# Optimization experiments

Measured on AMD Instinct MI355X. Metric: run time of the kernel, lower is better.

The kernel has to match this reference:

```python
import jax, jax.numpy as jnp
import numpy as np

D = 512
H = 8
DK = D // H
FF = 4 * D
EPS = 1e-5
NEG = -1.0e9


def _layernorm(x, g, b):
    mu = jnp.mean(x, axis=-1, keepdims=True)
    var = jnp.mean((x - mu) ** 2, axis=-1, keepdims=True)
    return (x - mu) * jax.lax.rsqrt(var + EPS) * g + b


def setup_inputs() -> dict:
    key = jax.random.key(0)
    ks = jax.random.split(key, 16)
    B, S = 4, 2048
    x = jax.random.normal(ks[0], (B, S, D), dtype=jnp.float32)
    # causal mask, broadcastable to [B, H, S, S]; mask==0 -> blocked
    mask = jnp.tril(jnp.ones((S, S), dtype=jnp.int32))[None, None]
    s = 1.0 / np.sqrt(D)
    sf = 1.0 / np.sqrt(FF)
    p = {
        "wq": jax.random.normal(ks[1], (D, D), jnp.float32) * s,
        "bq": jnp.zeros((D,), jnp.float32),
        "wk": jax.random.normal(ks[2], (D, D), jnp.float32) * s,
        "bk": jnp.zeros((D,), jnp.float32),
        "wv": jax.random.normal(ks[3], (D, D), jnp.float32) * s,
        "bv": jnp.zeros((D,), jnp.float32),
        "wo": jax.random.normal(ks[4], (D, D), jnp.float32) * s,
        "bo": jnp.zeros((D,), jnp.float32),
        "w1": jax.random.normal(ks[5], (D, FF), jnp.float32) * s,
        "b1": jnp.zeros((FF,), jnp.float32),
        "w2": jax.random.normal(ks[6], (FF, D), jnp.float32) * sf,
        "b2": jnp.zeros((D,), jnp.float32),
        "g1": jnp.ones((D,), jnp.float32),
        "be1": jnp.zeros((D,), jnp.float32),
        "g2": jnp.ones((D,), jnp.float32),
        "be2": jnp.zeros((D,), jnp.float32),
    }
    return {"x": x, "mask": mask, **p}


def reference(x, mask, wq, bq, wk, bk, wv, bv, wo, bo, w1, b1, w2, b2, g1, be1, g2, be2):
    B, S, _ = x.shape
    # projections -> [B, H, S, DK]
    q = (x @ wq + bq).reshape(B, S, H, DK).transpose(0, 2, 1, 3)
    k = (x @ wk + bk).reshape(B, S, H, DK).transpose(0, 2, 1, 3)
    v = (x @ wv + bv).reshape(B, S, H, DK).transpose(0, 2, 1, 3)
    scores = jnp.einsum("bhqd,bhkd->bhqk", q, k) / np.sqrt(DK)
    scores = jnp.where(mask == 0, NEG, scores)
    attn = jax.nn.softmax(scores, axis=-1)
    ctx = jnp.einsum("bhqk,bhkd->bhqd", attn, v)
    ctx = ctx.transpose(0, 2, 1, 3).reshape(B, S, D)
    attn_out = ctx @ wo + bo
    # dropout is inference-mode identity
    h = _layernorm(x + attn_out, g1, be1)
    ffn = jax.nn.relu(h @ w1 + b1) @ w2 + b2
    return _layernorm(h + ffn, g2, be2)
```

## Files before the change

### kernel.cpp

```cpp
#include <hip/hip_runtime.h>
#include <math.h>

#define D_   512
#define H_   8
#define DK_  64
#define FF_  2048
#define S_   2048
#define B_   4
#define M_   (B_*S_)
#define EPS_ 1e-5f
#define SCLQ 0.1803368801111f

typedef __attribute__((ext_vector_type(8))) short bf16x8;
typedef __attribute__((ext_vector_type(4))) short bf16x4;
typedef __attribute__((ext_vector_type(4))) float f32x4;
typedef __attribute__((ext_vector_type(4))) unsigned int u32x4;

__device__ inline unsigned short f2b(float f) {
    unsigned u = __builtin_bit_cast(unsigned, f);
    unsigned r = (u + 0x7FFFu + ((u >> 16) & 1u)) >> 16;
    return (unsigned short)r;
}
__device__ inline float b2f(unsigned short u) {
    return __builtin_bit_cast(float, (unsigned)u << 16);
}
__device__ inline unsigned packbf(float p0, float p1) {
    unsigned r;
    asm("v_cvt_pk_bf16_f32 %0, %1, %2" : "=v"(r) : "v"(p0), "v"(p1));
    return r;
}

__device__ __forceinline__ void async_cp16(const void* g, void* l) {
    __builtin_amdgcn_global_load_lds(
        (const __attribute__((address_space(1))) unsigned int*)g,
        (__attribute__((address_space(3))) unsigned int*)l, 16, 0, 0);
}

__global__ __launch_bounds__(256)
void prep_kernel(const float* __restrict__ x,
                 const float* __restrict__ wq, const float* __restrict__ wk,
                 const float* __restrict__ wv, const float* __restrict__ wo,
                 const float* __restrict__ bq, const float* __restrict__ bk,
                 const float* __restrict__ bv,
                 const float* __restrict__ w1, const float* __restrict__ w2,
                 unsigned short* __restrict__ xb, unsigned short* __restrict__ wqkvt,
                 unsigned short* __restrict__ wot, unsigned short* __restrict__ w1t,
                 unsigned short* __restrict__ w2t, float* __restrict__ bqkv)
{
    __shared__ float L[32][33];
    const int bid = blockIdx.x;
    const int tid = threadIdx.x;

    if (bid < 2048) {
        const int i = (bid * 256 + tid) * 8;
        const float4 a = *(const float4*)(x + i);
        const float4 b = *(const float4*)(x + i + 4);
        bf16x8 v;
        v[0] = (short)f2b(a.x); v[1] = (short)f2b(a.y);
        v[2] = (short)f2b(a.z); v[3] = (short)f2b(a.w);
        v[4] = (short)f2b(b.x); v[5] = (short)f2b(b.y);
        v[6] = (short)f2b(b.z); v[7] = (short)f2b(b.w);
        *(bf16x8*)(xb + i) = v;
        return;
    }

    const float* w; unsigned short* wt; int K, N, k0, n0; float scl = 1.f;
    if (bid < 3072) {
        const int z = (bid - 2048) >> 8;
        const int r = (bid - 2048) & 255;
        n0 = (r & 15) * 32; k0 = (r >> 4) * 32; K = 512; N = 512;
        w  = (z == 0) ? wq : (z == 1) ? wk : (z == 2) ? wv : wo;
        wt = (z < 3) ? (wqkvt + (size_t)z * 512 * 512) : wot;
        if (z == 0) scl = SCLQ;
        if (z < 3 && r == 0) {
            const float* bsrc = (z == 0) ? bq : (z == 1) ? bk : bv;
            const float bscl  = (z == 0) ? SCLQ : 1.f;
            bqkv[z * 512 + tid]       = bsrc[tid] * bscl;
            bqkv[z * 512 + 256 + tid] = bsrc[256 + tid] * bscl;
        }
    } else if (bid < 4096) {
        const int r = bid - 3072;
        n0 = (r & 63) * 32; k0 = (r >> 6) * 32; K = 512; N = 2048;
        w = w1; wt = w1t;
    } else {
        const int r = bid - 4096;
        n0 = (r & 15) * 32; k0 = (r >> 4) * 32; K = 2048; N = 512;
        w = w2; wt = w2t;
    }

    const int xx = tid & 31, y = tid >> 5;
#pragma unroll
    for (int i = 0; i < 4; i++)
        L[y + i * 8][xx] = w[(size_t)(k0 + y + i * 8) * N + n0 + xx] * scl;
    __syncthreads();
#pragma unroll
    for (int i = 0; i < 4; i++)
        wt[(size_t)(n0 + y + i * 8) * K + k0 + xx] = f2b(L[xx][y + i * 8]);
}

template<int WR, int WC, int MT, int NT, int BK, int OUTB, int RELU, int RESADD, int HASBIAS, int VT>
__global__ __launch_bounds__(256)
void gemm_bf16(const unsigned short* __restrict__ A, const unsigned short* __restrict__ Bt,
               const float* __restrict__ bias, const void* __restrict__ RES,
               void* __restrict__ Cv, unsigned short* __restrict__ vtout,
               int K, int lda, int ldb, int ldc)
{
    constexpr int BM  = WR * MT * 16;
    constexpr int BN  = WC * NT * 16;
    constexpr int CPR = BK / 8;
    constexpr int CA  = BM * BK / (256 * 8);
    constexpr int CB  = BN * BK / (256 * 8);
    __shared__ unsigned short As[2][BM * BK];
    __shared__ unsigned short Bs[2][BN * BK];

    const int tid  = threadIdx.x;
    const int lane = tid & 63;
    const int w    = tid >> 6;
    const int wr   = w / WC, wc = w % WC;
    const int quad = lane >> 4;
    const int l15  = lane & 15;

    const int nwg = gridDim.x * gridDim.y;
    const int lin = blockIdx.y * gridDim.x + blockIdx.x;
    const int swz = (lin & 7) * (nwg >> 3) + (lin >> 3);
    const int n0  = (swz % gridDim.x) * BN;
    const int m0  = (swz / gridDim.x) * BM;

    f32x4 acc[MT][NT];
#pragma unroll
    for (int i = 0; i < MT; i++)
#pragma unroll
        for (int j = 0; j < NT; j++) acc[i][j] = (f32x4){0.f, 0.f, 0.f, 0.f};

    auto stage = [&](int k0, int bufi) {
#pragma unroll
        for (int i = 0; i < CA; i++) {
            const int c   = tid + i * 256;
            const int row = c / CPR;
            int l = c % CPR;
            if (BK == 64) l ^= (row & 7);
            async_cp16(&A[(size_t)(m0 + row) * lda + k0 + l * 8], &As[bufi][c * 8]);
        }
#pragma unroll
        for (int i = 0; i < CB; i++) {
            const int c   = tid + i * 256;
            const int row = c / CPR;
            int l = c % CPR;
            if (BK == 64) l ^= (row & 7);
            async_cp16(&Bt[(size_t)(n0 + row) * ldb + k0 + l * 8], &Bs[bufi][c * 8]);
        }
    };

    stage(0, 0);
    const int niter = K / BK;
    for (int ii = 0; ii < niter; ii++) {
        const int knext = (ii + 1 < niter) ? (ii + 1) * BK : 0;
        stage(knext, (ii + 1) & 1);
        __builtin_amdgcn_s_waitcnt(0x0f70 | (CA + CB));
        __builtin_amdgcn_s_barrier();

        const unsigned short* Ac = &As[ii & 1][0];
        const unsigned short* Bc = &Bs[ii & 1][0];
#pragma unroll
        for (int ks = 0; ks < BK / 32; ks++) {
            bf16x8 af[MT], bfr[NT];
#pragma unroll
            for (int t = 0; t < MT; t++) {
                const int r = wr * MT * 16 + t * 16 + l15;
                int ch = (ks << 2) | quad;
                if (BK == 64) ch ^= (r & 7);
                af[t] = *(const bf16x8*)&Ac[r * BK + ch * 8];
            }
#pragma unroll
            for (int t = 0; t < NT; t++) {
                const int r = wc * NT * 16 + t * 16 + l15;
                int ch = (ks << 2) | quad;
                if (BK == 64) ch ^= (r & 7);
                bfr[t] = *(const bf16x8*)&Bc[r * BK + ch * 8];
            }
#pragma unroll
            for (int mt = 0; mt < MT; mt++)
#pragma unroll
                for (int nt = 0; nt < NT; nt++)
                    acc[mt][nt] = __builtin_amdgcn_mfma_f32_16x16x32_bf16(
                        af[mt], bfr[nt], acc[mt][nt], 0, 0, 0);
        }
        __builtin_amdgcn_s_barrier();
    }

#pragma unroll
    for (int mt = 0; mt < MT; mt++) {
        const int rowb = m0 + wr * MT * 16 + mt * 16 + quad * 4;
#pragma unroll
        for (int nt = 0; nt < NT; nt++) {
            const int col = n0 + wc * NT * 16 + nt * 16 + l15;
            const float bv = HASBIAS ? bias[col] : 0.f;
            if (VT && col >= 1024) {
                short4 sv;
                sv.x = (short)f2b(acc[mt][nt][0] + bv);
                sv.y = (short)f2b(acc[mt][nt][1] + bv);
                sv.z = (short)f2b(acc[mt][nt][2] + bv);
                sv.w = (short)f2b(acc[mt][nt][3] + bv);
                const int bb = rowb >> 11;
                *(short4*)&vtout[(size_t)(bb * 512 + (col - 1024)) * S_ + (rowb & 2047)] = sv;
            } else {
#pragma unroll
                for (int r = 0; r < 4; r++) {
                    const size_t idx = (size_t)(rowb + r) * ldc + col;
                    float v = acc[mt][nt][r] + bv;
                    if (RESADD == 1) v += ((const float*)RES)[idx];
                    if (RESADD == 2) v += b2f(((const unsigned short*)RES)[idx]);
                    if (RELU)   v = fmaxf(v, 0.f);
                    if (OUTB) ((unsigned short*)Cv)[idx] = f2b(v);
                    else      ((float*)Cv)[idx] = v;
                }
            }
        }
    }
}

__global__ __launch_bounds__(256, 4)
void attn_mfma(const unsigned short* __restrict__ qkv,
               const unsigned short* __restrict__ vt,
               unsigned short* __restrict__ ctx)
{
    __shared__ unsigned short Arena[16384];

    const int tid  = threadIdx.x;
    const int lane = tid & 63;
    const int w    = tid >> 6;
    const int quad = lane >> 4;
    const int l15  = lane & 15;
    const int bid  = blockIdx.x;
    const int g    = bid >> 5;
    const int qb   = (g < 8) ? 31 - g : (g < 16) ? g + 8 : (g < 24) ? 31 - g : g - 24;
    const int bh   = bid & 31;
    const int b    = bh >> 3, hh = bh & 7;
    const int kh   = w & 1;
    const int qh   = w >> 1;

    const unsigned short* qbase = qkv + (size_t)(b * S_) * 1536 + hh * 64;
    const unsigned short* kbase = qbase + 512;
    const unsigned short* vtb   = vt + (size_t)bh * 64 * S_;

    bf16x4 ones4;
#pragma unroll
    for (int j = 0; j < 4; j++) ones4[j] = (short)0x3F80;

    auto stage = [&](int kb, int bufi) {
        unsigned short* kd = &Arena[bufi * 4096];
        unsigned short* vd = &Arena[8192 + bufi * 4096];
#pragma unroll
        for (int i = 0; i < 2; i++) {
            const int c = tid + i * 256;
            const int row = c >> 3;
            const int l = (c & 7) ^ (row & 7);
            async_cp16(kbase + (size_t)(kb * 64 + row) * 1536 + l * 8, kd + c * 8);
            async_cp16(vtb + (size_t)row * S_ + kb * 64 + l * 8, vd + c * 8);
        }
    };

    bf16x8 qf[2][2];
#pragma unroll
    for (int qt = 0; qt < 2; qt++) {
        const unsigned short* qr = qbase + (size_t)(qb * 64 + qh * 32 + qt * 16 + l15) * 1536;
        qf[qt][0] = *(const bf16x8*)(qr + quad * 8);
        qf[qt][1] = *(const bf16x8*)(qr + 32 + quad * 8);
    }

    f32x4 Oacc[2][5];
#pragma unroll
    for (int qt = 0; qt < 2; qt++)
#pragma unroll
        for (int i = 0; i < 5; i++) Oacc[qt][i] = (f32x4){0.f, 0.f, 0.f, 0.f};

    stage(0, 0);

    const int vch0 = (kh * 4 + (quad >> 1));
    const int vsub = (quad & 1) * 4;

    for (int kb = 0; kb < qb; kb++) {
        stage(kb + 1, (kb + 1) & 1);
        __builtin_amdgcn_s_waitcnt(0x0F74);
        __builtin_amdgcn_s_barrier();
        const unsigned short* Kc = &Arena[(kb & 1) * 4096];
        const unsigned short* Vc = &Arena[8192 + (kb & 1) * 4096];

        f32x4 st[2][2];
#pragma unroll
        for (int qt = 0; qt < 2; qt++)
#pragma unroll
            for (int kt = 0; kt < 2; kt++) st[qt][kt] = (f32x4){0.f, 0.f, 0.f, 0.f};
#pragma unroll
        for (int kc = 0; kc < 2; kc++) {
            const int phys = (kc * 4 + quad) ^ (l15 & 7);
            const bf16x8 kf0 = *(const bf16x8*)&Kc[(kh * 32 + l15) * 64 + phys * 8];
            const bf16x8 kf1 = *(const bf16x8*)&Kc[(kh * 32 + 16 + l15) * 64 + phys * 8];
#pragma unroll
            for (int qt = 0; qt < 2; qt++) {
                st[qt][0] = __builtin_amdgcn_mfma_f32_16x16x32_bf16(kf0, qf[qt][kc], st[qt][0], 0, 0, 0);
                st[qt][1] = __builtin_amdgcn_mfma_f32_16x16x32_bf16(kf1, qf[qt][kc], st[qt][1], 0, 0, 0);
            }
        }

        bf16x4 vf[2][4];
#pragma unroll
        for (int kt = 0; kt < 2; kt++)
#pragma unroll
            for (int nt = 0; nt < 4; nt++)
                vf[kt][nt] = *(const bf16x4*)&Vc[(nt * 16 + l15) * 64 +
                    (((vch0 + kt * 2) ^ (l15 & 7)) << 3) + vsub];

#pragma unroll
        for (int qt = 0; qt < 2; qt++) {
#pragma unroll
            for (int kt = 0; kt < 2; kt++) {
                uint2 aw;
                aw.x = packbf(exp2f(st[qt][kt][0]), exp2f(st[qt][kt][1]));
                aw.y = packbf(exp2f(st[qt][kt][2]), exp2f(st[qt][kt][3]));
                const bf16x4 af = __builtin_bit_cast(bf16x4, aw);
#pragma unroll
                for (int nt = 0; nt < 4; nt++)
                    Oacc[qt][nt] = __builtin_amdgcn_mfma_f32_16x16x16bf16_1k(
                        af, vf[kt][nt], Oacc[qt][nt], 0, 0, 0);
                Oacc[qt][4] = __builtin_amdgcn_mfma_f32_16x16x16bf16_1k(
                    af, ones4, Oacc[qt][4], 0, 0, 0);
            }
        }
        __builtin_amdgcn_s_barrier();
    }

    {
        stage(0, (qb + 1) & 1);
        __builtin_amdgcn_s_waitcnt(0x0F74);
        __builtin_amdgcn_s_barrier();
        const unsigned short* Kc = &Arena[(qb & 1) * 4096];
        const unsigned short* Vc = &Arena[8192 + (qb & 1) * 4096];

        const bool skipDiag = (kh == 1 && qh == 0);
        const bool fullDiag = (kh == 0 && qh == 1);

        if (!skipDiag) {
            f32x4 st[2][2];
#pragma unroll
            for (int qt = 0; qt < 2; qt++)
#pragma unroll
                for (int kt = 0; kt < 2; kt++) st[qt][kt] = (f32x4){0.f, 0.f, 0.f, 0.f};
#pragma unroll
            for (int kc = 0; kc < 2; kc++) {
                const int phys = (kc * 4 + quad) ^ (l15 & 7);
                const bf16x8 kf0 = *(const bf16x8*)&Kc[(kh * 32 + l15) * 64 + phys * 8];
                const bf16x8 kf1 = *(const bf16x8*)&Kc[(kh * 32 + 16 + l15) * 64 + phys * 8];
#pragma unroll
                for (int qt = 0; qt < 2; qt++) {
                    st[qt][0] = __builtin_amdgcn_mfma_f32_16x16x32_bf16(kf0, qf[qt][kc], st[qt][0], 0, 0, 0);
                    st[qt][1] = __builtin_amdgcn_mfma_f32_16x16x32_bf16(kf1, qf[qt][kc], st[qt][1], 0, 0, 0);
                }
            }

            bf16x4 af[2][2];
            if (fullDiag) {
#pragma unroll
                for (int qt = 0; qt < 2; qt++)
#pragma unroll
                    for (int kt = 0; kt < 2; kt++) {
                        uint2 aw;
                        aw.x = packbf(exp2f(st[qt][kt][0]), exp2f(st[qt][kt][1]));
                        aw.y = packbf(exp2f(st[qt][kt][2]), exp2f(st[qt][kt][3]));
                        af[qt][kt] = __builtin_bit_cast(bf16x4, aw);
                    }
            } else {
                float p[4];
                uint2 aw;
#pragma unroll
                for (int r = 0; r < 4; r++)
                    p[r] = (quad * 4 + r > l15) ? 0.f : exp2f(st[0][0][r]);
                aw.x = packbf(p[0], p[1]); aw.y = packbf(p[2], p[3]);
                af[0][0] = __builtin_bit_cast(bf16x4, aw);
                af[0][1] = (bf16x4){0, 0, 0, 0};
                aw.x = packbf(exp2f(st[1][0][0]), exp2f(st[1][0][1]));
                aw.y = packbf(exp2f(st[1][0][2]), exp2f(st[1][0][3]));
                af[1][0] = __builtin_bit_cast(bf16x4, aw);
#pragma unroll
                for (int r = 0; r < 4; r++)
                    p[r] = (quad * 4 + r > l15) ? 0.f : exp2f(st[1][1][r]);
                aw.x = packbf(p[0], p[1]); aw.y = packbf(p[2], p[3]);
                af[1][1] = __builtin_bit_cast(bf16x4, aw);
            }

            bf16x4 vf[2][4];
#pragma unroll
            for (int kt = 0; kt < 2; kt++)
#pragma unroll
                for (int nt = 0; nt < 4; nt++)
                    vf[kt][nt] = *(const bf16x4*)&Vc[(nt * 16 + l15) * 64 +
                        (((vch0 + kt * 2) ^ (l15 & 7)) << 3) + vsub];

#pragma unroll
            for (int qt = 0; qt < 2; qt++)
#pragma unroll
                for (int kt = 0; kt < 2; kt++) {
#pragma unroll
                    for (int nt = 0; nt < 4; nt++)
                        Oacc[qt][nt] = __builtin_amdgcn_mfma_f32_16x16x16bf16_1k(
                            af[qt][kt], vf[kt][nt], Oacc[qt][nt], 0, 0, 0);
                    Oacc[qt][4] = __builtin_amdgcn_mfma_f32_16x16x16bf16_1k(
                        af[qt][kt], ones4, Oacc[qt][4], 0, 0, 0);
                }
        }
    }

    __syncthreads();
    float* red = (float*)&Arena[0];
    const int rbase = (qh * 64 + lane) * 44;
    if (kh) {
#pragma unroll
        for (int qt = 0; qt < 2; qt++)
#pragma unroll
            for (int i = 0; i < 5; i++)
                *(f32x4*)&red[rbase + (qt * 5 + i) * 4] = Oacc[qt][i];
    }
    __syncthreads();
    if (!kh) {
#pragma unroll
        for (int qt = 0; qt < 2; qt++)
#pragma unroll
            for (int i = 0; i < 5; i++)
                Oacc[qt][i] += *(const f32x4*)&red[rbase + (qt * 5 + i) * 4];

        unsigned short* cb = ctx + (size_t)(b * S_) * 512 + hh * 64;
#pragma unroll
        for (int qt = 0; qt < 2; qt++) {
            const int orow = qb * 64 + qh * 32 + qt * 16 + quad * 4;
#pragma unroll
            for (int r = 0; r < 4; r++) {
                const float inv = 1.f / Oacc[qt][4][r];
#pragma unroll
                for (int nt = 0; nt < 4; nt++)
                    cb[(size_t)(orow + r) * 512 + nt * 16 + l15] = f2b(Oacc[qt][nt][r] * inv);
            }
        }
    }
}

template<int WF, int WB>
__global__ __launch_bounds__(256)
void ln_kernel(const float* __restrict__ s, const float* __restrict__ g,
               const float* __restrict__ be, float* __restrict__ out,
               unsigned short* __restrict__ outb)
{
    const int wave = threadIdx.x >> 6;
    const int lane = threadIdx.x & 63;
    const int row  = blockIdx.x * 4 + wave;
    const float* ps = s + (size_t)row * D_;
    const int c0 = lane * 4;

    float v[8];
    {
        const float4 a0 = *(const float4*)(ps + c0);
        const float4 a1 = *(const float4*)(ps + c0 + 256);
        v[0] = a0.x; v[1] = a0.y; v[2] = a0.z; v[3] = a0.w;
        v[4] = a1.x; v[5] = a1.y; v[6] = a1.z; v[7] = a1.w;
    }

    float sum = 0.f;
#pragma unroll
    for (int i = 0; i < 8; i++) sum += v[i];
#pragma unroll
    for (int m = 1; m < 64; m <<= 1) sum += __shfl_xor(sum, m);
    const float mu = sum * (1.f / D_);

    float sq = 0.f;
#pragma unroll
    for (int i = 0; i < 8; i++) { const float d = v[i] - mu; sq += d * d; }
#pragma unroll
    for (int m = 1; m < 64; m <<= 1) sq += __shfl_xor(sq, m);
    const float rstd = rsqrtf(sq * (1.f / D_) + EPS_);

    const float4 g0 = *(const float4*)(g + c0);
    const float4 b0 = *(const float4*)(be + c0);
    const float4 g1 = *(const float4*)(g + c0 + 256);
    const float4 b1 = *(const float4*)(be + c0 + 256);

    float o[8];
    o[0] = (v[0] - mu) * rstd * g0.x + b0.x;
    o[1] = (v[1] - mu) * rstd * g0.y + b0.y;
    o[2] = (v[2] - mu) * rstd * g0.z + b0.z;
    o[3] = (v[3] - mu) * rstd * g0.w + b0.w;
    o[4] = (v[4] - mu) * rstd * g1.x + b1.x;
    o[5] = (v[5] - mu) * rstd * g1.y + b1.y;
    o[6] = (v[6] - mu) * rstd * g1.z + b1.z;
    o[7] = (v[7] - mu) * rstd * g1.w + b1.w;

    if (WF) {
        *(float4*)(out + (size_t)row * D_ + c0)       = *(float4*)&o[0];
        *(float4*)(out + (size_t)row * D_ + c0 + 256) = *(float4*)&o[4];
    }
    if (WB) {
        short4 vb0 = (short4){(short)f2b(o[0]), (short)f2b(o[1]), (short)f2b(o[2]), (short)f2b(o[3])};
        short4 vb1 = (short4){(short)f2b(o[4]), (short)f2b(o[5]), (short)f2b(o[6]), (short)f2b(o[7])};
        *(short4*)(outb + (size_t)row * D_ + c0)       = vb0;
        *(short4*)(outb + (size_t)row * D_ + c0 + 256) = vb1;
    }
}

extern "C" void kernel_launch(void* const* d_in, const int* in_sizes, int n_in,
                              void* d_out, int out_size, void* d_ws, size_t ws_size,
                              hipStream_t stream)
{
    const float* x  = (const float*)d_in[0];
    const float* wq = (const float*)d_in[2];
    const float* bq = (const float*)d_in[3];
    const float* wk = (const float*)d_in[4];
    const float* bk = (const float*)d_in[5];
    const float* wv = (const float*)d_in[6];
    const float* bv = (const float*)d_in[7];
    const float* wo = (const float*)d_in[8];
    const float* bo = (const float*)d_in[9];
    const float* w1 = (const float*)d_in[10];
    const float* b1 = (const float*)d_in[11];
    const float* w2 = (const float*)d_in[12];
    const float* b2 = (const float*)d_in[13];
    const float* g1 = (const float*)d_in[14];
    const float* be1= (const float*)d_in[15];
    const float* g2 = (const float*)d_in[16];
    const float* be2= (const float*)d_in[17];
    float* out = (float*)d_out;

    const size_t MB = 1048576;
    char* w8 = (char*)d_ws;
    unsigned short* wqkvt = (unsigned short*)(w8 + 0);
    unsigned short* wot   = (unsigned short*)(w8 + 1572864);
    unsigned short* w1t   = (unsigned short*)(w8 + 2097152);
    unsigned short* w2t   = (unsigned short*)(w8 + 4194304);
    float*          bqkv  = (float*)(w8 + 6291456);
    unsigned short* qkv   = (unsigned short*)(w8 + 8 * MB);
    unsigned short* ffn1b = qkv;
    unsigned short* xb    = (unsigned short*)(w8 + 40 * MB);
    unsigned short* ctx   = xb;
    unsigned short* vt    = (unsigned short*)(w8 + 48 * MB);
    unsigned short* hb    = vt;
    float*          pre   = (float*)(w8 + 56 * MB);

    const dim3 blk(256);

    prep_kernel<<<dim3(5120), blk, 0, stream>>>(
        x, wq, wk, wv, wo, bq, bk, bv, w1, w2, xb, wqkvt, wot, w1t, w2t, bqkv);

    gemm_bf16<2,2,2,4,64,1,0,0,1,1><<<dim3(12, 128), blk, 0, stream>>>(
        xb, wqkvt, bqkv, nullptr, qkv, vt, 512, 512, 512, 1536);

    attn_mfma<<<dim3(1024), blk, 0, stream>>>(qkv, vt, ctx);

    gemm_bf16<2,2,2,4,64,0,0,1,1,0><<<dim3(4, 128), blk, 0, stream>>>(
        ctx, wot, bo, x, pre, nullptr, 512, 512, 512, 512);

    ln_kernel<0,1><<<dim3(M_ / 4), blk, 0, stream>>>(pre, g1, be1, nullptr, hb);

    gemm_bf16<2,2,2,4,64,1,1,0,1,0><<<dim3(16, 128), blk, 0, stream>>>(
        hb, w1t, b1, nullptr, ffn1b, nullptr, 512, 512, 512, 2048);

    gemm_bf16<2,2,2,4,64,0,0,2,1,0><<<dim3(4, 128), blk, 0, stream>>>(
        ffn1b, w2t, b2, hb, pre, nullptr, 2048, 2048, 2048, 512);

    ln_kernel<1,0><<<dim3(M_ / 4), blk, 0, stream>>>(pre, g2, be2, out, nullptr);
}
```

Measured before the change: 250.0 us.

## Split-K the FFN2 GEMM in two and fold partials, bias, residual into LayerNorm

The FFN down-projection (K=2048) is split into two K halves launched as a z-dimension of the grid, each writing raw fp32 partial sums to a separate buffer. The final LayerNorm kernel reads both partials, adds the bias and the bf16 residual, then normalizes. This doubles the block count of a GEMM that had only 512 workgroups, to fill more compute units. The cost is an extra fp32 write and read of an M×512 tensor plus moving the epilogue work into LayerNorm.

```diff
diff --git a/kernel.cpp b/kernel.cpp
--- a/kernel.cpp
+++ b/kernel.cpp
@@ -98,11 +98,12 @@
         wt[(size_t)(n0 + y + i * 8) * K + k0 + xx] = f2b(L[xx][y + i * 8]);
 }
 
-template<int WR, int WC, int MT, int NT, int BK, int OUTB, int RELU, int RESADD, int HASBIAS, int VT>
+template<int WR, int WC, int MT, int NT, int BK, int OUTB, int RELU, int RESADD, int HASBIAS, int VT, int SPLITK>
 __global__ __launch_bounds__(256)
 void gemm_bf16(const unsigned short* __restrict__ A, const unsigned short* __restrict__ Bt,
                const float* __restrict__ bias, const void* __restrict__ RES,
                void* __restrict__ Cv, unsigned short* __restrict__ vtout,
+               float* __restrict__ Cv2,
                int K, int lda, int ldb, int ldc)
 {
     constexpr int BM  = WR * MT * 16;
@@ -125,6 +126,7 @@
     const int swz = (lin & 7) * (nwg >> 3) + (lin >> 3);
     const int n0  = (swz % gridDim.x) * BN;
     const int m0  = (swz / gridDim.x) * BM;
+    const int koff = SPLITK ? blockIdx.z * K : 0;
 
     f32x4 acc[MT][NT];
 #pragma unroll
@@ -139,7 +141,7 @@
             const int row = c / CPR;
             int l = c % CPR;
             if (BK == 64) l ^= (row & 7);
-            async_cp16(&A[(size_t)(m0 + row) * lda + k0 + l * 8], &As[bufi][c * 8]);
+            async_cp16(&A[(size_t)(m0 + row) * lda + koff + k0 + l * 8], &As[bufi][c * 8]);
         }
 #pragma unroll
         for (int i = 0; i < CB; i++) {
@@ -147,7 +149,7 @@
             const int row = c / CPR;
             int l = c % CPR;
             if (BK == 64) l ^= (row & 7);
-            async_cp16(&Bt[(size_t)(n0 + row) * ldb + k0 + l * 8], &Bs[bufi][c * 8]);
+            async_cp16(&Bt[(size_t)(n0 + row) * ldb + koff + k0 + l * 8], &Bs[bufi][c * 8]);
         }
     };
 
@@ -194,6 +196,13 @@
 #pragma unroll
         for (int nt = 0; nt < NT; nt++) {
             const int col = n0 + wc * NT * 16 + nt * 16 + l15;
+            if (SPLITK) {
+                float* dst = blockIdx.z ? Cv2 : (float*)Cv;
+#pragma unroll
+                for (int r = 0; r < 4; r++)
+                    dst[(size_t)(rowb + r) * ldc + col] = acc[mt][nt][r];
+                continue;
+            }
             const float bv = HASBIAS ? bias[col] : 0.f;
             if (VT && col >= 1024) {
                 short4 sv;
@@ -443,11 +452,13 @@
     }
 }
 
-template<int WF, int WB>
+template<int WF, int WB, int COMB>
 __global__ __launch_bounds__(256)
 void ln_kernel(const float* __restrict__ s, const float* __restrict__ g,
                const float* __restrict__ be, float* __restrict__ out,
-               unsigned short* __restrict__ outb)
+               unsigned short* __restrict__ outb,
+               const float* __restrict__ s2, const unsigned short* __restrict__ resb,
+               const float* __restrict__ bias2)
 {
     const int wave = threadIdx.x >> 6;
     const int lane = threadIdx.x & 63;
@@ -461,6 +472,23 @@
         const float4 a1 = *(const float4*)(ps + c0 + 256);
         v[0] = a0.x; v[1] = a0.y; v[2] = a0.z; v[3] = a0.w;
         v[4] = a1.x; v[5] = a1.y; v[6] = a1.z; v[7] = a1.w;
+    }
+    if (COMB) {
+        const float* ps2 = s2 + (size_t)row * D_;
+        const float4 c00 = *(const float4*)(ps2 + c0);
+        const float4 c1 = *(const float4*)(ps2 + c0 + 256);
+        const float4 bb0 = *(const float4*)(bias2 + c0);
+        const float4 bb1 = *(const float4*)(bias2 + c0 + 256);
+        const short4 r0 = *(const short4*)(resb + (size_t)row * D_ + c0);
+        const short4 r1 = *(const short4*)(resb + (size_t)row * D_ + c0 + 256);
+        v[0] += c00.x + bb0.x + b2f((unsigned short)r0.x);
+        v[1] += c00.y + bb0.y + b2f((unsigned short)r0.y);
+        v[2] += c00.z + bb0.z + b2f((unsigned short)r0.z);
+        v[3] += c00.w + bb0.w + b2f((unsigned short)r0.w);
+        v[4] += c1.x + bb1.x + b2f((unsigned short)r1.x);
+        v[5] += c1.y + bb1.y + b2f((unsigned short)r1.y);
+        v[6] += c1.z + bb1.z + b2f((unsigned short)r1.z);
+        v[7] += c1.w + bb1.w + b2f((unsigned short)r1.w);
     }
 
     float sum = 0.f;
@@ -541,27 +569,30 @@
     unsigned short* vt    = (unsigned short*)(w8 + 48 * MB);
     unsigned short* hb    = vt;
     float*          pre   = (float*)(w8 + 56 * MB);
+    float*          pre2  = (float*)(w8 + 72 * MB);
 
     const dim3 blk(256);
 
     prep_kernel<<<dim3(5120), blk, 0, stream>>>(
         x, wq, wk, wv, wo, bq, bk, bv, w1, w2, xb, wqkvt, wot, w1t, w2t, bqkv);
 
-    gemm_bf16<2,2,2,4,64,1,0,0,1,1><<<dim3(12, 128), blk, 0, stream>>>(
-        xb, wqkvt, bqkv, nullptr, qkv, vt, 512, 512, 512, 1536);
+    gemm_bf16<2,2,2,4,64,1,0,0,1,1,0><<<dim3(12, 128), blk, 0, stream>>>(
+        xb, wqkvt, bqkv, nullptr, qkv, vt, nullptr, 512, 512, 512, 1536);
 
     attn_mfma<<<dim3(1024), blk, 0, stream>>>(qkv, vt, ctx);
 
-    gemm_bf16<2,2,2,4,64,0,0,1,1,0><<<dim3(4, 128), blk, 0, stream>>>(
-        ctx, wot, bo, x, pre, nullptr, 512, 512, 512, 512);
-
-    ln_kernel<0,1><<<dim3(M_ / 4), blk, 0, stream>>>(pre, g1, be1, nullptr, hb);
-
-    gemm_bf16<2,2,2,4,64,1,1,0,1,0><<<dim3(16, 128), blk, 0, stream>>>(
-        hb, w1t, b1, nullptr, ffn1b, nullptr, 512, 512, 512, 2048);
-
-    gemm_bf16<2,2,2,4,64,0,0,2,1,0><<<dim3(4, 128), blk, 0, stream>>>(
-        ffn1b, w2t, b2, hb, pre, nullptr, 2048, 2048, 2048, 512);
-
-    ln_kernel<1,0><<<dim3(M_ / 4), blk, 0, stream>>>(pre, g2, be2, out, nullptr);
-}
+    gemm_bf16<2,2,2,4,64,0,0,1,1,0,0><<<dim3(4, 128), blk, 0, stream>>>(
+        ctx, wot, bo, x, pre, nullptr, nullptr, 512, 512, 512, 512);
+
+    ln_kernel<0,1,0><<<dim3(M_ / 4), blk, 0, stream>>>(
+        pre, g1, be1, nullptr, hb, nullptr, nullptr, nullptr);
+
+    gemm_bf16<2,2,2,4,64,1,1,0,1,0,0><<<dim3(16, 128), blk, 0, stream>>>(
+        hb, w1t, b1, nullptr, ffn1b, nullptr, nullptr, 512, 512, 512, 2048);
+
+    gemm_bf16<2,2,2,4,64,0,0,0,0,0,1><<<dim3(4, 128, 2), blk, 0, stream>>>(
+        ffn1b, w2t, nullptr, nullptr, pre, nullptr, pre2, 1024, 2048, 2048, 512);
+
+    ln_kernel<1,0,1><<<dim3(M_ / 4), blk, 0, stream>>>(
+        pre, g2, be2, out, nullptr, pre2, hb, b2);
+}
```

Measured after the change: 254.1 us. About the same (+1.6%).
